# Performance work log

Measured on AMD Instinct MI355X. Metric: run time of the kernel, lower is better.

The kernel has to match this reference:

```python
import jax, jax.numpy as jnp
import numpy as np

N, OBS, H, M, L = 512, 32, 128, 128, 3


def _w(key, shape, fan_in):
    return jax.random.normal(key, shape, dtype=jnp.float32) / np.sqrt(fan_in)


def setup_inputs() -> dict:
    key = jax.random.key(0)
    ks = iter(jax.random.split(key, 64))
    inp = {}
    inp["obs"] = jax.random.normal(next(ks), (N, OBS), dtype=jnp.float32)
    inp["pos"] = jax.random.uniform(next(ks), (N, 2), dtype=jnp.float32)
    # encoder: obs_dim -> H -> H -> H
    inp["enc_W1"] = _w(next(ks), (H, OBS), OBS); inp["enc_b1"] = jnp.zeros((H,), jnp.float32)
    inp["enc_W2"] = _w(next(ks), (H, H), H);     inp["enc_b2"] = jnp.zeros((H,), jnp.float32)
    inp["enc_W3"] = _w(next(ks), (H, H), H);     inp["enc_b3"] = jnp.zeros((H,), jnp.float32)
    # per-layer message MLPs: (2H+1) -> M -> M -> M, stacked over L layers
    inp["msg_W1"] = _w(next(ks), (L, M, 2 * H + 1), 2 * H + 1); inp["msg_b1"] = jnp.zeros((L, M), jnp.float32)
    inp["msg_W2"] = _w(next(ks), (L, M, M), M);                 inp["msg_b2"] = jnp.zeros((L, M), jnp.float32)
    inp["msg_W3"] = _w(next(ks), (L, M, M), M);                 inp["msg_b3"] = jnp.zeros((L, M), jnp.float32)
    # per-layer update MLPs: (H+M) -> H -> H -> H, stacked over L layers
    inp["upd_W1"] = _w(next(ks), (L, H, H + M), H + M); inp["upd_b1"] = jnp.zeros((L, H), jnp.float32)
    inp["upd_W2"] = _w(next(ks), (L, H, H), H);         inp["upd_b2"] = jnp.zeros((L, H), jnp.float32)
    inp["upd_W3"] = _w(next(ks), (L, H, H), H);         inp["upd_b3"] = jnp.zeros((L, H), jnp.float32)
    return inp


def _mlp3(x, W1, b1, W2, b2, W3, b3):
    h = jax.nn.relu(x @ W1.T + b1)
    h = jax.nn.relu(h @ W2.T + b2)
    return h @ W3.T + b3


def reference(obs, pos, enc_W1, enc_b1, enc_W2, enc_b2, enc_W3, enc_b3,
              msg_W1, msg_b1, msg_W2, msg_b2, msg_W3, msg_b3,
              upd_W1, upd_b1, upd_W2, upd_b2, upd_W3, upd_b3):
    n = obs.shape[0]
    h = enc_W1.shape[0]
    z = _mlp3(obs, enc_W1, enc_b1, enc_W2, enc_b2, enc_W3, enc_b3)  # (N, H)
    # pairwise distances; guard diagonal sqrt(0) for grad safety, then zero it
    diff = pos[:, None, :] - pos[None, :, :]                  # (N, N, 2)
    sq = jnp.sum(diff * diff, axis=-1)                        # (N, N)
    eye = jnp.eye(n, dtype=pos.dtype)
    dist = jnp.sqrt(jnp.where(eye > 0, 1.0, sq)) * (1.0 - eye)
    nondiag = (1.0 - eye)[:, :, None]
    n_layers = msg_W1.shape[0]
    for l in range(n_layers):
        W1 = msg_W1[l]
        Wi, Wj, wd = W1[:, :h], W1[:, h:2 * h], W1[:, 2 * h]  # split concat [z_i, z_j, d]
        A = z @ Wi.T                                          # (N, M) receiver term
        B = z @ Wj.T                                          # (N, M) sender term
        h1 = jax.nn.relu(A[:, None, :] + B[None, :, :] + dist[:, :, None] * wd + msg_b1[l])  # (N, N, M)
        h2 = jax.nn.relu(jnp.einsum('ijm,km->ijk', h1, msg_W2[l]) + msg_b2[l])
        m = jnp.einsum('ijm,km->ijk', h2, msg_W3[l]) + msg_b3[l]
        m = m * nondiag                                       # exclude j == i
        msum = jnp.sum(m, axis=1)                             # (N, M) sum over senders j
        z = _mlp3(jnp.concatenate([z, msum], axis=-1),
                  upd_W1[l], upd_b1[l], upd_W2[l], upd_b2[l], upd_W3[l], upd_b3[l])
    return z
```

## Files before the change

### kernel.cpp

```cpp
#include <hip/hip_runtime.h>

#define NA 512
#define NOBS 32
#define NH 128

typedef const float* fp32p;
typedef __attribute__((ext_vector_type(8))) short bf16x8;
typedef __attribute__((ext_vector_type(4))) float f32x4;

__device__ __forceinline__ unsigned cvt_pk_bf16(float lo, float hi) {
    unsigned r;
    asm("v_cvt_pk_bf16_f32 %0, %1, %2" : "=v"(r) : "v"(lo), "v"(hi));
    return r;
}

__device__ __forceinline__ bf16x8 wfrag_f4(const float* p) {
    float4 u = *(const float4*)p;
    float4 v = *(const float4*)(p + 4);
    union { unsigned w[4]; bf16x8 f; } r;
    r.w[0] = cvt_pk_bf16(u.x, u.y);
    r.w[1] = cvt_pk_bf16(u.z, u.w);
    r.w[2] = cvt_pk_bf16(v.x, v.y);
    r.w[3] = cvt_pk_bf16(v.z, v.w);
    return r.f;
}

#define HSTR 136

__global__ __launch_bounds__(512) void enc_ab_kernel(
    fp32p obs, fp32p eW1, fp32p eb1, fp32p eW2, fp32p eb2, fp32p eW3, fp32p eb3,
    fp32p mW1, float* __restrict__ z, float* __restrict__ A, float* __restrict__ B) {
    const int i = blockIdx.x;
    const int t = threadIdx.x;
    const int nn = t >> 2;
    const int ks = t & 3;

    __shared__ float xs0[NOBS];
    __shared__ float part[4 * NH];
    __shared__ float part2[4 * NH];
    __shared__ float hx[NH], hy[NH], zz[NH];

    if (t < NOBS) xs0[t] = obs[(size_t)i * NOBS + t];
    __syncthreads();
    {
        const float* wr = eW1 + (size_t)nn * NOBS + ks * 8;
        const float4 w0 = *(const float4*)wr;
        const float4 w1 = *(const float4*)(wr + 4);
        const float4 x0 = *(const float4*)&xs0[ks * 8];
        const float4 x1 = *(const float4*)&xs0[ks * 8 + 4];
        part[ks * NH + nn] = w0.x * x0.x + w0.y * x0.y + w0.z * x0.z + w0.w * x0.w +
                             w1.x * x1.x + w1.y * x1.y + w1.z * x1.z + w1.w * x1.w;
    }
    __syncthreads();
    if (t < NH)
        hx[t] = fmaxf(eb1[t] + part[t] + part[NH + t] + part[2 * NH + t] + part[3 * NH + t], 0.f);
    __syncthreads();
    {
        const float* wr = eW2 + (size_t)nn * NH + ks * 4;
        float p = 0.f;
        #pragma unroll
        for (int it = 0; it < 8; ++it) {
            const float4 wv = *(const float4*)(wr + it * 16);
            const float4 xv = *(const float4*)&hx[it * 16 + ks * 4];
            p += wv.x * xv.x + wv.y * xv.y + wv.z * xv.z + wv.w * xv.w;
        }
        part[ks * NH + nn] = p;
    }
    __syncthreads();
    if (t < NH)
        hy[t] = fmaxf(eb2[t] + part[t] + part[NH + t] + part[2 * NH + t] + part[3 * NH + t], 0.f);
    __syncthreads();
    {
        const float* wr = eW3 + (size_t)nn * NH + ks * 4;
        float p = 0.f;
        #pragma unroll
        for (int it = 0; it < 8; ++it) {
            const float4 wv = *(const float4*)(wr + it * 16);
            const float4 xv = *(const float4*)&hy[it * 16 + ks * 4];
            p += wv.x * xv.x + wv.y * xv.y + wv.z * xv.z + wv.w * xv.w;
        }
        part[ks * NH + nn] = p;
    }
    __syncthreads();
    if (t < NH) {
        const float v = eb3[t] + part[t] + part[NH + t] + part[2 * NH + t] + part[3 * NH + t];
        z[(size_t)i * NH + t] = v;
        zz[t] = v;
    }
    __syncthreads();
    {
        const float* pr = mW1 + (size_t)nn * 257;
        float pa = 0.f, pb = 0.f;
        #pragma unroll
        for (int it = 0; it < 8; ++it) {
            #pragma unroll
            for (int j = 0; j < 4; ++j) {
                const int k = it * 16 + ks * 4 + j;
                const float x = zz[k];
                pa += x * pr[k];
                pb += x * pr[NH + k];
            }
        }
        part[ks * NH + nn] = pa;
        part2[ks * NH + nn] = pb;
    }
    __syncthreads();
    if (t < NH) {
        A[(size_t)i * NH + t] = part[t] + part[NH + t] + part[2 * NH + t] + part[3 * NH + t];
        B[(size_t)i * NH + t] = part2[t] + part2[NH + t] + part2[2 * NH + t] + part2[3 * NH + t];
    }
}

__global__ __launch_bounds__(512) void msg_upd_kernel(
    const float* __restrict__ A, const float* __restrict__ B,
    fp32p pos, const float* __restrict__ zin,
    fp32p W1l, fp32p b1, fp32p W2, fp32p b2, fp32p W3, fp32p b3,
    fp32p uW1, fp32p ub1, fp32p uW2, fp32p ub2, fp32p uW3, fp32p ub3,
    fp32p msgW1n, int do_ab,
    float* __restrict__ zout, float* __restrict__ An, float* __restrict__ Bn) {
    const int i = blockIdx.x;
    const int t = threadIdx.x;
    const int lane = t & 63;
    const int w = t >> 6;
    const int q = lane >> 4;
    const int c = lane & 15;
    const int ncol = w * 16 + c;

    __shared__ short h1s[128 * HSTR];
    __shared__ short h2s[128 * HSTR];
    __shared__ float distrow[NA];
    __shared__ float amrow[NH];
    __shared__ float wdsr[NH];
    __shared__ float xs2[2 * NH];
    __shared__ float part[4 * NH];
    __shared__ float part2[4 * NH];
    __shared__ float hx[NH], hy[NH], hz[NH];

    if (t < NH) {
        amrow[t] = A[i * NH + t] + b1[t];
        wdsr[t]  = W1l[t * 257 + 256];
        xs2[t] = zin[(size_t)i * NH + t];
    }
    {
        const float2 pi = *(const float2*)&pos[2 * i];
        const float2 pj = *(const float2*)&pos[2 * t];
        const float dx = pi.x - pj.x, dy = pi.y - pj.y;
        const float s = dx * dx + dy * dy;
        distrow[t] = (t == i) ? 0.0f : sqrtf(s);
    }

    bf16x8 w2f[4], w3f[4];
    {
        const float* w2r = W2 + (size_t)ncol * NH + q * 8;
        const float* w3r = W3 + (size_t)ncol * NH + q * 8;
        #pragma unroll
        for (int kb = 0; kb < 4; ++kb) {
            w2f[kb] = wfrag_f4(w2r + kb * 32);
            w3f[kb] = wfrag_f4(w3r + kb * 32);
        }
    }
    const float b2n = b2[ncol];

    const int m2 = lane * 2;
    float psum = 0.0f;

    __syncthreads();
    const float am0 = amrow[m2], am1 = amrow[m2 + 1];
    const float wd0 = wdsr[m2],  wd1 = wdsr[m2 + 1];

#define BUILD(c4_) do {                                                      \
        const int j0_ = (c4_) * 128;                                         \
        _Pragma("unroll")                                                    \
        for (int rr = 0; rr < 16; ++rr) {                                    \
            const int row_ = rr * 8 + w;                                     \
            const int jg_ = j0_ + row_;                                      \
            const float2 bv_ = *(const float2*)&B[(size_t)jg_ * NH + m2];    \
            const float d_ = distrow[jg_];                                   \
            const float v0_ = fmaxf(fmaf(d_, wd0, am0 + bv_.x), 0.0f);       \
            const float v1_ = fmaxf(fmaf(d_, wd1, am1 + bv_.y), 0.0f);       \
            *(unsigned*)&h1s[row_ * HSTR + m2] = cvt_pk_bf16(v0_, v1_);      \
        }                                                                    \
    } while (0)

#define GEMM1() do {                                                         \
        _Pragma("unroll")                                                    \
        for (int jt = 0; jt < 8; ++jt) {                                     \
            f32x4 acc = {0.f, 0.f, 0.f, 0.f};                                \
            const short* arow = &h1s[(jt * 16 + c) * HSTR + q * 8];          \
            _Pragma("unroll")                                                \
            for (int kb = 0; kb < 4; ++kb) {                                 \
                bf16x8 a = *(const bf16x8*)(arow + kb * 32);                 \
                acc = __builtin_amdgcn_mfma_f32_16x16x32_bf16(a, w2f[kb], acc, 0, 0, 0); \
            }                                                                \
            const int orow = jt * 16 + q * 4;                                \
            const unsigned p01 = cvt_pk_bf16(fmaxf(acc[0] + b2n, 0.0f),      \
                                             fmaxf(acc[1] + b2n, 0.0f));     \
            const unsigned p23 = cvt_pk_bf16(fmaxf(acc[2] + b2n, 0.0f),      \
                                             fmaxf(acc[3] + b2n, 0.0f));     \
            const unsigned send = (c & 1) ? p01 : p23;                       \
            const unsigned recv = __shfl_xor(send, 1, 64);                   \
            const unsigned keep = (c & 1) ? p23 : p01;                       \
            const unsigned lo = (c & 1) ? recv : keep;                       \
            const unsigned hi = (c & 1) ? keep : recv;                       \
            const unsigned d0 = (lo & 0xFFFFu) | (hi << 16);                 \
            const unsigned d1 = (lo >> 16) | (hi & 0xFFFF0000u);             \
            const int rbase = orow + ((c & 1) << 1);                         \
            const int colb = ncol & ~1;                                      \
            *(unsigned*)&h2s[(rbase + 0) * HSTR + colb] = d0;                \
            *(unsigned*)&h2s[(rbase + 1) * HSTR + colb] = d1;                \
        }                                                                    \
    } while (0)

#define GEMM2(c4_) do {                                                      \
        const int j0_ = (c4_) * 128;                                         \
        _Pragma("unroll")                                                    \
        for (int jt = 0; jt < 8; ++jt) {                                     \
            f32x4 acc = {0.f, 0.f, 0.f, 0.f};                                \
            const short* arow = &h2s[(jt * 16 + c) * HSTR + q * 8];          \
            _Pragma("unroll")                                                \
            for (int kb = 0; kb < 4; ++kb) {                                 \
                bf16x8 a = *(const bf16x8*)(arow + kb * 32);                 \
                acc = __builtin_amdgcn_mfma_f32_16x16x32_bf16(a, w3f[kb], acc, 0, 0, 0); \
            }                                                                \
            _Pragma("unroll")                                                \
            for (int r = 0; r < 4; ++r) {                                    \
                const int jg_ = j0_ + jt * 16 + q * 4 + r;                   \
                if (jg_ != i) psum += acc[r];                                \
            }                                                                \
        }                                                                    \
    } while (0)

    BUILD(0);
    __syncthreads();
    GEMM1();
    for (int c4 = 0; c4 < 4; ++c4) {
        __syncthreads();
        if (c4 < 3) {
            BUILD(c4 + 1);
            GEMM2(c4);
            __syncthreads();
            GEMM1();
        } else {
            GEMM2(c4);
        }
    }
#undef BUILD
#undef GEMM1
#undef GEMM2

    psum += __shfl_xor(psum, 16, 64);
    psum += __shfl_xor(psum, 32, 64);
    if (lane < 16) xs2[NH + ncol] = psum + 511.0f * b3[ncol];
    __syncthreads();

    const int nn = t >> 2;
    const int ks = t & 3;
    {
        const float* wr = uW1 + (size_t)nn * 256 + ks * 4;
        float p = 0.f;
        #pragma unroll
        for (int it = 0; it < 16; ++it) {
            const float4 wv = *(const float4*)(wr + it * 16);
            const float4 xv = *(const float4*)&xs2[it * 16 + ks * 4];
            p += wv.x * xv.x + wv.y * xv.y + wv.z * xv.z + wv.w * xv.w;
        }
        part[ks * NH + nn] = p;
    }
    __syncthreads();
    if (t < NH)
        hx[t] = fmaxf(ub1[t] + part[t] + part[NH + t] + part[2 * NH + t] + part[3 * NH + t], 0.f);
    __syncthreads();
    {
        const float* wr = uW2 + (size_t)nn * NH + ks * 4;
        float p = 0.f;
        #pragma unroll
        for (int it = 0; it < 8; ++it) {
            const float4 wv = *(const float4*)(wr + it * 16);
            const float4 xv = *(const float4*)&hx[it * 16 + ks * 4];
            p += wv.x * xv.x + wv.y * xv.y + wv.z * xv.z + wv.w * xv.w;
        }
        part[ks * NH + nn] = p;
    }
    __syncthreads();
    if (t < NH)
        hy[t] = fmaxf(ub2[t] + part[t] + part[NH + t] + part[2 * NH + t] + part[3 * NH + t], 0.f);
    __syncthreads();
    {
        const float* wr = uW3 + (size_t)nn * NH + ks * 4;
        float p = 0.f;
        #pragma unroll
        for (int it = 0; it < 8; ++it) {
            const float4 wv = *(const float4*)(wr + it * 16);
            const float4 xv = *(const float4*)&hy[it * 16 + ks * 4];
            p += wv.x * xv.x + wv.y * xv.y + wv.z * xv.z + wv.w * xv.w;
        }
        part[ks * NH + nn] = p;
    }
    __syncthreads();
    if (t < NH) {
        const float v = ub3[t] + part[t] + part[NH + t] + part[2 * NH + t] + part[3 * NH + t];
        zout[(size_t)i * NH + t] = v;
        hz[t] = v;
    }
    if (!do_ab) return;
    __syncthreads();
    {
        const float* pr = msgW1n + (size_t)nn * 257;
        float pa = 0.f, pb = 0.f;
        #pragma unroll
        for (int it = 0; it < 8; ++it) {
            #pragma unroll
            for (int j = 0; j < 4; ++j) {
                const int k = it * 16 + ks * 4 + j;
                const float x = hz[k];
                pa += x * pr[k];
                pb += x * pr[NH + k];
            }
        }
        part[ks * NH + nn] = pa;
        part2[ks * NH + nn] = pb;
    }
    __syncthreads();
    if (t < NH) {
        An[(size_t)i * NH + t] = part[t] + part[NH + t] + part[2 * NH + t] + part[3 * NH + t];
        Bn[(size_t)i * NH + t] = part2[t] + part2[NH + t] + part2[2 * NH + t] + part2[3 * NH + t];
    }
}

extern "C" void kernel_launch(void* const* d_in, const int* in_sizes, int n_in,
                              void* d_out, int out_size, void* d_ws, size_t ws_size,
                              hipStream_t stream) {
    fp32p obs   = (fp32p)d_in[0];
    fp32p pos   = (fp32p)d_in[1];
    fp32p encW1 = (fp32p)d_in[2];  fp32p encb1 = (fp32p)d_in[3];
    fp32p encW2 = (fp32p)d_in[4];  fp32p encb2 = (fp32p)d_in[5];
    fp32p encW3 = (fp32p)d_in[6];  fp32p encb3 = (fp32p)d_in[7];
    fp32p msgW1 = (fp32p)d_in[8];  fp32p msgb1 = (fp32p)d_in[9];
    fp32p msgW2 = (fp32p)d_in[10]; fp32p msgb2 = (fp32p)d_in[11];
    fp32p msgW3 = (fp32p)d_in[12]; fp32p msgb3 = (fp32p)d_in[13];
    fp32p updW1 = (fp32p)d_in[14]; fp32p updb1 = (fp32p)d_in[15];
    fp32p updW2 = (fp32p)d_in[16]; fp32p updb2 = (fp32p)d_in[17];
    fp32p updW3 = (fp32p)d_in[18]; fp32p updb3 = (fp32p)d_in[19];

    float* ws = (float*)d_ws;
    float* zA = ws;
    float* zB = zA + NA * NH;
    float* A0 = zB + NA * NH;
    float* B0 = A0 + NA * NH;
    float* A1 = B0 + NA * NH;
    float* B1 = A1 + NA * NH;

    enc_ab_kernel<<<NA, 512, 0, stream>>>(obs, encW1, encb1, encW2, encb2,
                                          encW3, encb3, msgW1, zA, A0, B0);

    float* zin = zA;  float* zout = zB;
    float* Ac = A0;   float* Bc = B0;
    float* An = A1;   float* Bn = B1;
    for (int l = 0; l < 3; ++l) {
        const int do_ab = (l < 2);
        float* dst = (l == 2) ? (float*)d_out : zout;
        msg_upd_kernel<<<NA, 512, 0, stream>>>(Ac, Bc, pos, zin,
            msgW1 + (size_t)l * 128 * 257, msgb1 + l * 128,
            msgW2 + (size_t)l * 128 * 128, msgb2 + l * 128,
            msgW3 + (size_t)l * 128 * 128, msgb3 + l * 128,
            updW1 + (size_t)l * 256 * 128, updb1 + l * 128,
            updW2 + (size_t)l * 128 * 128, updb2 + l * 128,
            updW3 + (size_t)l * 128 * 128, updb3 + l * 128,
            msgW1 + (size_t)(l + 1 < 3 ? l + 1 : 0) * 128 * 257, do_ab,
            dst, An, Bn);
        float* tmp;
        tmp = zin; zin = zout; zout = tmp;
        tmp = Ac; Ac = An; An = tmp;
        tmp = Bc; Bc = Bn; Bn = tmp;
    }
}
```

Measured before the change: 210.0 us.

## Batch encoder over 16 nodes per block using bf16 MFMA

Rewrites the encoder and A/B projection kernel so each block handles 16 nodes and computes all four matmuls with bf16 16x16x32 MFMA instructions instead of per-node scalar FP32 dot products with shared-memory partial reductions. This amortizes weight loads across 16 rows and cuts the grid from 512 to 32 blocks. Intermediate activations are now rounded to bf16, which adds precision error to z, A and B. The smaller grid also leaves most compute units idle during the encoder.

```diff
diff --git a/kernel.cpp b/kernel.cpp
--- a/kernel.cpp
+++ b/kernel.cpp
@@ -25,89 +25,98 @@
     return r.f;
 }
 
+__device__ __forceinline__ bf16x8 wfrag_s(const float* p) {
+    union { unsigned w[4]; bf16x8 f; } r;
+    r.w[0] = cvt_pk_bf16(p[0], p[1]);
+    r.w[1] = cvt_pk_bf16(p[2], p[3]);
+    r.w[2] = cvt_pk_bf16(p[4], p[5]);
+    r.w[3] = cvt_pk_bf16(p[6], p[7]);
+    return r.f;
+}
+
 #define HSTR 136
 
 __global__ __launch_bounds__(512) void enc_ab_kernel(
     fp32p obs, fp32p eW1, fp32p eb1, fp32p eW2, fp32p eb2, fp32p eW3, fp32p eb3,
     fp32p mW1, float* __restrict__ z, float* __restrict__ A, float* __restrict__ B) {
-    const int i = blockIdx.x;
+    const int i0 = blockIdx.x * 16;
     const int t = threadIdx.x;
-    const int nn = t >> 2;
-    const int ks = t & 3;
-
-    __shared__ float xs0[NOBS];
-    __shared__ float part[4 * NH];
-    __shared__ float part2[4 * NH];
-    __shared__ float hx[NH], hy[NH], zz[NH];
-
-    if (t < NOBS) xs0[t] = obs[(size_t)i * NOBS + t];
-    __syncthreads();
-    {
-        const float* wr = eW1 + (size_t)nn * NOBS + ks * 8;
-        const float4 w0 = *(const float4*)wr;
-        const float4 w1 = *(const float4*)(wr + 4);
-        const float4 x0 = *(const float4*)&xs0[ks * 8];
-        const float4 x1 = *(const float4*)&xs0[ks * 8 + 4];
-        part[ks * NH + nn] = w0.x * x0.x + w0.y * x0.y + w0.z * x0.z + w0.w * x0.w +
-                             w1.x * x1.x + w1.y * x1.y + w1.z * x1.z + w1.w * x1.w;
-    }
-    __syncthreads();
-    if (t < NH)
-        hx[t] = fmaxf(eb1[t] + part[t] + part[NH + t] + part[2 * NH + t] + part[3 * NH + t], 0.f);
-    __syncthreads();
-    {
-        const float* wr = eW2 + (size_t)nn * NH + ks * 4;
-        float p = 0.f;
-        #pragma unroll
-        for (int it = 0; it < 8; ++it) {
-            const float4 wv = *(const float4*)(wr + it * 16);
-            const float4 xv = *(const float4*)&hx[it * 16 + ks * 4];
-            p += wv.x * xv.x + wv.y * xv.y + wv.z * xv.z + wv.w * xv.w;
-        }
-        part[ks * NH + nn] = p;
-    }
-    __syncthreads();
-    if (t < NH)
-        hy[t] = fmaxf(eb2[t] + part[t] + part[NH + t] + part[2 * NH + t] + part[3 * NH + t], 0.f);
-    __syncthreads();
-    {
-        const float* wr = eW3 + (size_t)nn * NH + ks * 4;
-        float p = 0.f;
-        #pragma unroll
-        for (int it = 0; it < 8; ++it) {
-            const float4 wv = *(const float4*)(wr + it * 16);
-            const float4 xv = *(const float4*)&hy[it * 16 + ks * 4];
-            p += wv.x * xv.x + wv.y * xv.y + wv.z * xv.z + wv.w * xv.w;
-        }
-        part[ks * NH + nn] = p;
-    }
-    __syncthreads();
-    if (t < NH) {
-        const float v = eb3[t] + part[t] + part[NH + t] + part[2 * NH + t] + part[3 * NH + t];
-        z[(size_t)i * NH + t] = v;
-        zz[t] = v;
-    }
-    __syncthreads();
-    {
-        const float* pr = mW1 + (size_t)nn * 257;
-        float pa = 0.f, pb = 0.f;
-        #pragma unroll
-        for (int it = 0; it < 8; ++it) {
-            #pragma unroll
-            for (int j = 0; j < 4; ++j) {
-                const int k = it * 16 + ks * 4 + j;
-                const float x = zz[k];
-                pa += x * pr[k];
-                pb += x * pr[NH + k];
-            }
-        }
-        part[ks * NH + nn] = pa;
-        part2[ks * NH + nn] = pb;
-    }
-    __syncthreads();
-    if (t < NH) {
-        A[(size_t)i * NH + t] = part[t] + part[NH + t] + part[2 * NH + t] + part[3 * NH + t];
-        B[(size_t)i * NH + t] = part2[t] + part2[NH + t] + part2[2 * NH + t] + part2[3 * NH + t];
+    const int lane = t & 63;
+    const int w = t >> 6;
+    const int q = lane >> 4;
+    const int c = lane & 15;
+    const int q8 = q * 8;
+    const int ncol = w * 16 + c;
+
+    __shared__ short ha[16 * HSTR];
+    __shared__ short hb[16 * HSTR];
+
+    {
+        const bf16x8 af = wfrag_f4(obs + (size_t)(i0 + c) * NOBS + q8);
+        const bf16x8 bf = wfrag_f4(eW1 + (size_t)ncol * NOBS + q8);
+        f32x4 acc = {0.f, 0.f, 0.f, 0.f};
+        acc = __builtin_amdgcn_mfma_f32_16x16x32_bf16(af, bf, acc, 0, 0, 0);
+        const float bn = eb1[ncol];
+        #pragma unroll
+        for (int r = 0; r < 4; ++r) {
+            const float v = fmaxf(acc[r] + bn, 0.f);
+            ha[(q * 4 + r) * HSTR + ncol] = (short)cvt_pk_bf16(v, v);
+        }
+    }
+    __syncthreads();
+    {
+        f32x4 acc = {0.f, 0.f, 0.f, 0.f};
+        const short* ar = &ha[c * HSTR + q8];
+        #pragma unroll
+        for (int kb = 0; kb < 4; ++kb) {
+            const bf16x8 a = *(const bf16x8*)(ar + kb * 32);
+            const bf16x8 b = wfrag_f4(eW2 + (size_t)ncol * NH + kb * 32 + q8);
+            acc = __builtin_amdgcn_mfma_f32_16x16x32_bf16(a, b, acc, 0, 0, 0);
+        }
+        const float bn = eb2[ncol];
+        #pragma unroll
+        for (int r = 0; r < 4; ++r) {
+            const float v = fmaxf(acc[r] + bn, 0.f);
+            hb[(q * 4 + r) * HSTR + ncol] = (short)cvt_pk_bf16(v, v);
+        }
+    }
+    __syncthreads();
+    {
+        f32x4 acc = {0.f, 0.f, 0.f, 0.f};
+        const short* ar = &hb[c * HSTR + q8];
+        #pragma unroll
+        for (int kb = 0; kb < 4; ++kb) {
+            const bf16x8 a = *(const bf16x8*)(ar + kb * 32);
+            const bf16x8 b = wfrag_f4(eW3 + (size_t)ncol * NH + kb * 32 + q8);
+            acc = __builtin_amdgcn_mfma_f32_16x16x32_bf16(a, b, acc, 0, 0, 0);
+        }
+        const float bn = eb3[ncol];
+        #pragma unroll
+        for (int r = 0; r < 4; ++r) {
+            const float v = acc[r] + bn;
+            z[(size_t)(i0 + q * 4 + r) * NH + ncol] = v;
+            ha[(q * 4 + r) * HSTR + ncol] = (short)cvt_pk_bf16(v, v);
+        }
+    }
+    __syncthreads();
+    {
+        f32x4 aa = {0.f, 0.f, 0.f, 0.f};
+        f32x4 ab = {0.f, 0.f, 0.f, 0.f};
+        const short* ar = &ha[c * HSTR + q8];
+        const float* wrow = mW1 + (size_t)ncol * 257;
+        #pragma unroll
+        for (int kb = 0; kb < 4; ++kb) {
+            const bf16x8 a = *(const bf16x8*)(ar + kb * 32);
+            const bf16x8 bi = wfrag_s(wrow + kb * 32 + q8);
+            const bf16x8 bj = wfrag_s(wrow + 128 + kb * 32 + q8);
+            aa = __builtin_amdgcn_mfma_f32_16x16x32_bf16(a, bi, aa, 0, 0, 0);
+            ab = __builtin_amdgcn_mfma_f32_16x16x32_bf16(a, bj, ab, 0, 0, 0);
+        }
+        #pragma unroll
+        for (int r = 0; r < 4; ++r) {
+            A[(size_t)(i0 + q * 4 + r) * NH + ncol] = aa[r];
+            B[(size_t)(i0 + q * 4 + r) * NH + ncol] = ab[r];
+        }
     }
 }
 
@@ -350,8 +359,8 @@
     float* A1 = B0 + NA * NH;
     float* B1 = A1 + NA * NH;
 
-    enc_ab_kernel<<<NA, 512, 0, stream>>>(obs, encW1, encb1, encW2, encb2,
-                                          encW3, encb3, msgW1, zA, A0, B0);
+    enc_ab_kernel<<<NA / 16, 512, 0, stream>>>(obs, encW1, encb1, encW2, encb2,
+                                               encW3, encb3, msgW1, zA, A0, B0);
 
     float* zin = zA;  float* zout = zB;
     float* Ac = A0;   float* Bc = B0;
```

New measurement: 207.8 us. No clear change (-1.1%).
